# Kernel tuning notes

Measured on AMD Instinct MI355X. Metric: run time of the kernel, lower is better.

Reference implementation:

```python
import jax, jax.numpy as jnp
import numpy as np

INPUT_SIZE = 224
B, C, H, W = 256, 3, 256, 256
KSIZE = 15
KHALF = KSIZE // 2


def setup_inputs() -> dict:
    key = jax.random.key(0)
    x = jax.random.uniform(key, (B, C, H, W), dtype=jnp.float32)
    return {"x": x}


def _rgb_to_hsv(img):  # img [B,3,Hs,Ws] -> (h,s,v) each [B,Hs,Ws]
    r, g, b = img[:, 0], img[:, 1], img[:, 2]
    maxc = jnp.maximum(jnp.maximum(r, g), b)
    minc = jnp.minimum(jnp.minimum(r, g), b)
    v = maxc
    d = maxc - minc
    s = jnp.where(maxc > 0, d / jnp.where(maxc > 0, maxc, 1.0), 0.0)
    dn = jnp.where(d > 0, d, 1.0)
    rc, gc, bc = (maxc - r) / dn, (maxc - g) / dn, (maxc - b) / dn
    h = jnp.where(maxc == r, bc - gc, jnp.where(maxc == g, 2.0 + rc - bc, 4.0 + gc - rc))
    h = jnp.where(d > 0, (h / 6.0) % 1.0, 0.0)
    return h, s, v


def _hsv_to_rgb(h, s, v):  # -> [B,3,Hs,Ws]
    i = jnp.floor(h * 6.0)
    f = h * 6.0 - i
    i = i.astype(jnp.int32) % 6
    p = v * (1.0 - s)
    q = v * (1.0 - s * f)
    t = v * (1.0 - s * (1.0 - f))
    conds = [i == 0, i == 1, i == 2, i == 3, i == 4, i == 5]
    r = jnp.select(conds, [v, q, p, p, t, v])
    g = jnp.select(conds, [t, v, v, q, p, p])
    b = jnp.select(conds, [p, p, t, v, v, q])
    return jnp.stack([r, g, b], axis=1)


def _gray(img):  # ITU-R 601 luma, keep channel dim
    w = jnp.array([0.2989, 0.587, 0.114], dtype=img.dtype).reshape(1, 3, 1, 1)
    return jnp.sum(img * w, axis=1, keepdims=True)


def _blur_axis(img, kern, axis):
    # img [B,C,S,S]; kern [B,KSIZE]; separable 1D gaussian along `axis` with reflect pad
    pad = [(0, 0)] * 4
    pad[axis] = (KHALF, KHALF)
    xp = jnp.pad(img, pad, mode='reflect')
    out = jnp.zeros_like(img)
    S = img.shape[axis]
    for k in range(KSIZE):  # fixed small loop, fuses under jit
        sl = jax.lax.slice_in_dim(xp, k, k + S, axis=axis)
        out = out + kern[:, k].reshape(B, 1, 1, 1) * sl
    return out


def _pipeline(x):
    key = jax.random.key(42)
    ks = jax.random.split(key, 10)

    # ---- RandomResizedCrop(scale=(0.8,1.0), ratio=(3/4,4/3), bicubic) ----
    area = (H * W) * jax.random.uniform(ks[0], (B,), minval=0.8, maxval=1.0)
    ratio = jnp.exp(jax.random.uniform(ks[1], (B,), minval=np.log(3.0 / 4.0), maxval=np.log(4.0 / 3.0)))
    cw = jnp.clip(jnp.round(jnp.sqrt(area * ratio)), 1.0, float(W))
    ch = jnp.clip(jnp.round(jnp.sqrt(area / ratio)), 1.0, float(H))
    i0 = jnp.floor(jax.random.uniform(ks[2], (B,)) * (H - ch + 1.0))
    j0 = jnp.floor(jax.random.uniform(ks[3], (B,)) * (W - cw + 1.0))
    sy, sx = INPUT_SIZE / ch, INPUT_SIZE / cw
    ty, tx = -i0 * sy, -j0 * sx

    def crop_resize(img, scale, trans):
        return jax.image.scale_and_translate(
            img, (C, INPUT_SIZE, INPUT_SIZE), (1, 2), scale, trans,
            method='cubic', antialias=True)

    xc = jax.vmap(crop_resize)(x, jnp.stack([sy, sx], -1), jnp.stack([ty, tx], -1))

    # ---- ColorJitter(0.1, 0.1, 0.1, 0.01), RandomApply p=0.8 ----
    bf = jax.random.uniform(ks[4], (B, 1, 1, 1), minval=0.9, maxval=1.1)
    cf = jax.random.uniform(ks[5], (B, 1, 1, 1), minval=0.9, maxval=1.1)
    sf = jax.random.uniform(ks[6], (B, 1, 1, 1), minval=0.9, maxval=1.1)
    hf = jax.random.uniform(ks[7], (B, 1, 1), minval=-0.01, maxval=0.01)

    xj = jnp.clip(xc * bf, 0.0, 1.0)                                      # brightness
    mean_gray = jnp.mean(_gray(xj), axis=(2, 3), keepdims=True)
    xj = jnp.clip(cf * xj + (1.0 - cf) * mean_gray, 0.0, 1.0)             # contrast
    xj = jnp.clip(sf * xj + (1.0 - sf) * _gray(xj), 0.0, 1.0)             # saturation
    h, s, v = _rgb_to_hsv(xj)                                             # hue
    xj = _hsv_to_rgb((h + hf) % 1.0, s, v)

    apply_cj = (jax.random.uniform(ks[8], (B, 1, 1, 1)) < 0.8)
    xj = jnp.where(apply_cj, xj, xc)

    # ---- GaussianBlur(kernel_size=15, sigma~U(0.1,2.0)), RandomApply p=0.5 ----
    kb = jax.random.split(ks[9], 2)
    sigma = jax.random.uniform(kb[0], (B,), minval=0.1, maxval=2.0)
    t = jnp.arange(KSIZE, dtype=jnp.float32) - KHALF
    kern = jnp.exp(-0.5 * (t[None, :] / sigma[:, None]) ** 2)
    kern = kern / jnp.sum(kern, axis=1, keepdims=True)                    # [B,15]
    xb = _blur_axis(_blur_axis(xj, kern, 2), kern, 3)
    apply_bl = (jax.random.uniform(kb[1], (B, 1, 1, 1)) < 0.5)
    return jnp.where(apply_bl, xb, xj)


def reference(x):
    return _pipeline(x)
```

## Files before the change

### kernel.cpp

```cpp
#include <hip/hip_runtime.h>
#include <cstdint>
#include <cstddef>


#define JAX_PARTITIONABLE 1

#define NB 256
#define NC 3
#define IH 256
#define IW 256
#define OS 224
#define PIX (OS * OS)
#define PSTRIDE 32
#define TROWS 16
#define LROWS 24
#define NTILE 14
#define CSTRIDE 28
#define YSTR 25

__device__ __forceinline__ float bf2f(unsigned short u) {
  return __uint_as_float(((unsigned)u) << 16);
}
__device__ __forceinline__ unsigned short f2bf(float f) {
  unsigned u = __float_as_uint(f);
  return (unsigned short)((u + 0x7FFFu + ((u >> 16) & 1u)) >> 16);
}

__device__ __forceinline__ void tf2x32(uint32_t k0, uint32_t k1,
                                       uint32_t x0, uint32_t x1,
                                       uint32_t& o0, uint32_t& o1) {
  uint32_t ks[3] = {k0, k1, k0 ^ k1 ^ 0x1BD11BDAu};
  uint32_t a = x0 + ks[0], b = x1 + ks[1];
  const int R[2][4] = {{13, 15, 26, 6}, {17, 29, 16, 24}};
  #pragma unroll
  for (int i = 0; i < 5; ++i) {
    #pragma unroll
    for (int j = 0; j < 4; ++j) {
      int r = R[i & 1][j];
      a += b;
      b = (b << r) | (b >> (32 - r));
      b ^= a;
    }
    a += ks[(i + 1) % 3];
    b += ks[(i + 2) % 3] + (uint32_t)(i + 1);
  }
  o0 = a; o1 = b;
}

__device__ __forceinline__ float bits_to_u01(uint32_t bits) {
  uint32_t fb = (bits >> 9) | 0x3f800000u;
  return __uint_as_float(fb) - 1.0f;
}

__device__ __forceinline__ float u01_n(uint32_t k0, uint32_t k1, uint32_t i, uint32_t N) {
#if JAX_PARTITIONABLE
  uint32_t a, b; tf2x32(k0, k1, 0u, i, a, b);
  return bits_to_u01(a ^ b);
#else
  uint32_t half = N >> 1;
  uint32_t a, b;
  if (i < half) { tf2x32(k0, k1, i, half + i, a, b); return bits_to_u01(a); }
  tf2x32(k0, k1, i - half, i, a, b); return bits_to_u01(b);
#endif
}

__device__ __forceinline__ float junif(uint32_t k0, uint32_t k1, uint32_t i, uint32_t N,
                                       float mn, float mx) {
  float u = u01_n(k0, k1, i, N);
  float d = __fsub_rn(mx, mn);
  float r = __fadd_rn(__fmul_rn(u, d), mn);
  return fmaxf(mn, r);
}

__global__ __launch_bounds__(256) void k_params(float* __restrict__ prm) {
  int b = threadIdx.x;
  if (b >= NB) return;
  uint32_t ks[10][2];
#if JAX_PARTITIONABLE
  for (int j = 0; j < 10; ++j) tf2x32(0u, 42u, 0u, (uint32_t)j, ks[j][0], ks[j][1]);
#else
  {
    uint32_t flat[20];
    for (int j = 0; j < 10; ++j) {
      uint32_t a, bb; tf2x32(0u, 42u, (uint32_t)j, (uint32_t)(10 + j), a, bb);
      flat[j] = a; flat[10 + j] = bb;
    }
    for (int j = 0; j < 10; ++j) { ks[j][0] = flat[2 * j]; ks[j][1] = flat[2 * j + 1]; }
  }
#endif
  float* P = prm + b * PSTRIDE;

  float uarea = junif(ks[0][0], ks[0][1], b, NB, 0.8f, 1.0f);
  float area  = __fmul_rn(65536.0f, uarea);
  float lmn = (float)(-0.28768207245178085);
  float lmx = (float)( 0.28768207245178085);
  float ur  = junif(ks[1][0], ks[1][1], b, NB, lmn, lmx);
  float ratio = (float)exp((double)ur);

  float cw = rintf(__fsqrt_rn(__fmul_rn(area, ratio)));
  cw = fminf(fmaxf(cw, 1.0f), 256.0f);
  float ch = rintf(__fsqrt_rn(__fdiv_rn(area, ratio)));
  ch = fminf(fmaxf(ch, 1.0f), 256.0f);

  float ui = u01_n(ks[2][0], ks[2][1], b, NB);
  float uj = u01_n(ks[3][0], ks[3][1], b, NB);
  float i0 = floorf(__fmul_rn(ui, __fadd_rn(__fsub_rn(256.0f, ch), 1.0f)));
  float j0 = floorf(__fmul_rn(uj, __fadd_rn(__fsub_rn(256.0f, cw), 1.0f)));

  float sy = __fdiv_rn(224.0f, ch), sx = __fdiv_rn(224.0f, cw);
  float ty = -__fmul_rn(i0, sy),   tx = -__fmul_rn(j0, sx);
  float inv_sy = __fdiv_rn(1.0f, sy), inv_sx = __fdiv_rn(1.0f, sx);
  P[0] = inv_sy;
  P[1] = __fmul_rn(ty, inv_sy);
  P[2] = fmaxf(inv_sy, 1.0f);
  P[3] = inv_sx;
  P[4] = __fmul_rn(tx, inv_sx);
  P[5] = fmaxf(inv_sx, 1.0f);

  P[6] = junif(ks[4][0], ks[4][1], b, NB, 0.9f, 1.1f);
  P[7] = junif(ks[5][0], ks[5][1], b, NB, 0.9f, 1.1f);
  P[8] = junif(ks[6][0], ks[6][1], b, NB, 0.9f, 1.1f);
  P[9] = junif(ks[7][0], ks[7][1], b, NB, -0.01f, 0.01f);
  P[10] = (u01_n(ks[8][0], ks[8][1], b, NB) < 0.8f) ? 1.0f : 0.0f;

  uint32_t kb0[2], kb1[2];
#if JAX_PARTITIONABLE
  tf2x32(ks[9][0], ks[9][1], 0u, 0u, kb0[0], kb0[1]);
  tf2x32(ks[9][0], ks[9][1], 0u, 1u, kb1[0], kb1[1]);
#else
  {
    uint32_t f0, s0, f1, s1;
    tf2x32(ks[9][0], ks[9][1], 0u, 2u, f0, s0);
    tf2x32(ks[9][0], ks[9][1], 1u, 3u, f1, s1);
    kb0[0] = f0; kb0[1] = f1; kb1[0] = s0; kb1[1] = s1;
  }
#endif
  float sg = junif(kb0[0], kb0[1], b, NB, 0.1f, 2.0f);
  P[11] = (u01_n(kb1[0], kb1[1], b, NB) < 0.5f) ? 1.0f : 0.0f;

  float e[15]; float ssum = 0.0f;
  for (int k = 0; k < 15; ++k) {
    float t = (float)k - 7.0f;
    float z = t / sg;
    e[k] = expf(-0.5f * (z * z));
    ssum += e[k];
  }
  for (int k = 0; k < 15; ++k) P[12 + k] = e[k] / ssum;
}

__device__ __forceinline__ float keys_cubic(float x) {
  float o = ((1.5f * x - 2.5f) * x) * x + 1.0f;
  if (x >= 1.0f) o = ((-0.5f * x + 2.5f) * x - 4.0f) * x + 2.0f;
  if (x >= 2.0f) o = 0.0f;
  return o;
}

__global__ __launch_bounds__(224) void k_weights(const float* __restrict__ prm,
                                                 float* __restrict__ wtab) {
  int o = threadIdx.x;
  int dim = blockIdx.x & 1;
  int b = blockIdx.x >> 1;
  const float* P = prm + b * PSTRIDE;
  float inv = dim ? P[3] : P[0];
  float ti  = dim ? P[4] : P[1];
  float ks  = dim ? P[5] : P[2];
  float sf = ((float)o + 0.5f) * inv - ti - 0.5f;
  float r = 2.0f * ks;
  int i0 = max(0, (int)ceilf(sf - r));
  int i1 = min(255, (int)floorf(sf + r));
  int n = i1 - i0 + 1; if (n > 6) n = 6;
  float w[6]; float tot = 0.0f;
  #pragma unroll
  for (int j = 0; j < 6; ++j) {
    float v = 0.0f;
    if (j < n) { float d = fabsf(sf - (float)(i0 + j)) / ks; v = keys_cubic(d); }
    w[j] = v; tot += v;
  }
  float ri = (fabsf(tot) > 1.1920929e-4f) ? (1.0f / tot) : 0.0f;
  float* W = wtab + ((size_t)(b * 2 + dim) * 224 + o) * 8;
  #pragma unroll
  for (int j = 0; j < 6; ++j) W[j] = w[j] * ri;
  W[6] = (float)i0;
  W[7] = (float)n;
}

__global__ __launch_bounds__(256) void k_resize(const float* __restrict__ x,
                                                unsigned short* __restrict__ xcj,
                                                float* __restrict__ rowsum,
                                                const float* __restrict__ prm,
                                                const float* __restrict__ wtab) {
  int blk = blockIdx.x;
  int tile = blk % NTILE;
  int c = (blk / NTILE) % NC;
  int b = blk / (NTILE * NC);
  int t = threadIdx.x;
  int oyb = tile * TROWS;
  const float* P = prm + b * PSTRIDE;
  const float* wty = wtab + ((size_t)(b * 2) * 224 + oyb) * 8;

  __shared__ __align__(16) float s_mem[256 * CSTRIDE];
  __shared__ __align__(16) float s_wyl[TROWS * 8];
  __shared__ float wsum[4];

  if (t < TROWS * 8) s_wyl[t] = wty[t];

  int base = (int)wty[6];

  {
    const float* src = x + (size_t)(b * NC + c) * IH * IW + t;
    float* colp = s_mem + t * CSTRIDE;
    #pragma unroll
    for (int k = 0; k < 6; ++k) {
      float4 v;
      v.x = src[(size_t)min(base + 4 * k + 0, IH - 1) * IW];
      v.y = src[(size_t)min(base + 4 * k + 1, IH - 1) * IW];
      v.z = src[(size_t)min(base + 4 * k + 2, IH - 1) * IW];
      v.w = src[(size_t)min(base + 4 * k + 3, IH - 1) * IW];
      *(float4*)(colp + 4 * k) = v;
    }
  }
  __syncthreads();

  float xr[LROWS];
  #pragma unroll
  for (int r = 0; r < LROWS; ++r) xr[r] = 0.0f;
  if (t < OS) {
    const float4* W4 = (const float4*)(wtab + ((size_t)(b * 2 + 1) * 224 + t) * 8);
    float4 wA = W4[0], wB = W4[1];
    int ix0 = (int)wB.z;
    #pragma unroll
    for (int j = 0; j < 6; ++j) {
      float wj = (j == 0) ? wA.x : (j == 1) ? wA.y : (j == 2) ? wA.z
               : (j == 3) ? wA.w : (j == 4) ? wB.x : wB.y;
      const float* colp = s_mem + (ix0 + j) * CSTRIDE;
      #pragma unroll
      for (int k = 0; k < 6; ++k) {
        float4 f = *(const float4*)(colp + 4 * k);
        xr[4 * k + 0] += wj * f.x;
        xr[4 * k + 1] += wj * f.y;
        xr[4 * k + 2] += wj * f.z;
        xr[4 * k + 3] += wj * f.w;
      }
    }
  }
  __syncthreads();

  {
    float* colq = s_mem + t * YSTR;
    #pragma unroll
    for (int r = 0; r < LROWS; ++r) colq[r] = xr[r];
  }
  __syncthreads();

  float bfac = P[6];
  float psum = 0.0f;
  bool act = (t < OS);
  unsigned short* dst = xcj + ((size_t)(b * NC + c) * OS + oyb) * OS + t;
  const float* colq = s_mem + t * YSTR;
  #pragma unroll 2
  for (int i = 0; i < TROWS; ++i) {
    float4 a = *(const float4*)&s_wyl[i * 8];
    float4 h = *(const float4*)&s_wyl[i * 8 + 4];
    int ry0 = (int)h.z - base;
    const float* p = colq + ry0;
    float acc = a.x * p[0] + a.y * p[1] + a.z * p[2]
              + a.w * p[3] + h.x * p[4] + h.y * p[5];
    if (act) {
      dst[(size_t)i * OS] = f2bf(acc);
      psum += fminf(fmaxf(acc * bfac, 0.0f), 1.0f);
    }
  }
  for (int off = 32; off > 0; off >>= 1) psum += __shfl_down(psum, off, 64);
  int wid = t >> 6, lane = t & 63;
  if (lane == 0) wsum[wid] = psum;
  __syncthreads();
  if (t == 0) rowsum[blk] = wsum[0] + wsum[1] + wsum[2] + wsum[3];
}

__global__ __launch_bounds__(64) void k_means(const float* __restrict__ rowsum,
                                              float* __restrict__ means) {
  int b = blockIdx.x, t = threadIdx.x;
  float acc = 0.0f;
  if (t < NC * NTILE) {
    int c = t / NTILE;
    float w = (c == 0) ? 0.2989f : ((c == 1) ? 0.587f : 0.114f);
    acc = w * rowsum[b * NC * NTILE + t];
  }
  for (int off = 32; off > 0; off >>= 1) acc += __shfl_down(acc, off, 64);
  if (t == 0) means[b] = acc / (float)PIX;
}

__device__ __forceinline__ float clip01(float x) { return fminf(fmaxf(x, 0.0f), 1.0f); }
__device__ __forceinline__ float fmod1(float x)  { return x - floorf(x); }

__device__ __forceinline__ void jitter_px(float& r, float& g, float& bb,
                                          float mg, float bfac, float cfac,
                                          float sfac, float hfac) {
  r = clip01(r * bfac); g = clip01(g * bfac); bb = clip01(bb * bfac);
  r  = clip01(cfac * r  + (1.0f - cfac) * mg);
  g  = clip01(cfac * g  + (1.0f - cfac) * mg);
  bb = clip01(cfac * bb + (1.0f - cfac) * mg);
  float gray = 0.2989f * r + 0.587f * g + 0.114f * bb;
  r  = clip01(sfac * r  + (1.0f - sfac) * gray);
  g  = clip01(sfac * g  + (1.0f - sfac) * gray);
  bb = clip01(sfac * bb + (1.0f - sfac) * gray);
  float maxc = fmaxf(r, fmaxf(g, bb));
  float minc = fminf(r, fminf(g, bb));
  float v = maxc, d = maxc - minc;
  float s = (maxc > 0.0f) ? (d / maxc) : 0.0f;
  float dn = (d > 0.0f) ? d : 1.0f;
  float rc = (maxc - r) / dn, gc = (maxc - g) / dn, bc2 = (maxc - bb) / dn;
  float h = (maxc == r) ? (bc2 - gc)
          : ((maxc == g) ? (2.0f + rc - bc2) : (4.0f + gc - rc));
  h = (d > 0.0f) ? fmod1(h / 6.0f) : 0.0f;
  h = fmod1(h + hfac);
  float fi = floorf(h * 6.0f);
  float f = h * 6.0f - fi;
  int i = ((int)fi) % 6;
  float pp = v * (1.0f - s);
  float q  = v * (1.0f - s * f);
  float tt = v * (1.0f - s * (1.0f - f));
  switch (i) {
    case 0: r = v;  g = tt; bb = pp; break;
    case 1: r = q;  g = v;  bb = pp; break;
    case 2: r = pp; g = v;  bb = tt; break;
    case 3: r = pp; g = q;  bb = v;  break;
    case 4: r = tt; g = pp; bb = v;  break;
    default: r = v; g = pp; bb = q;  break;
  }
}

__global__ __launch_bounds__(256) void k_jitter(unsigned short* __restrict__ xcj,
                                                const float* __restrict__ means,
                                                const float* __restrict__ prm,
                                                float* __restrict__ out) {
  int idx = blockIdx.x * 256 + threadIdx.x;
  const int QPB = PIX / 4;
  if (idx >= NB * QPB) return;
  int b = idx / QPB, p4 = idx - b * QPB;
  const float* P = prm + b * PSTRIDE;
  float bfac = P[6], cfac = P[7], sfac = P[8], hfac = P[9];
  bool cj = P[10] != 0.0f;
  bool bl = P[11] != 0.0f;
  if (bl && !cj) return;
  size_t base4 = ((size_t)b * NC * PIX) / 4 + p4;
  ushort4* in4 = (ushort4*)xcj;
  ushort4 ru = in4[base4];
  ushort4 gu = in4[base4 + PIX / 4];
  ushort4 bu = in4[base4 + 2 * (PIX / 4)];
  float4 r4 = make_float4(bf2f(ru.x), bf2f(ru.y), bf2f(ru.z), bf2f(ru.w));
  float4 g4 = make_float4(bf2f(gu.x), bf2f(gu.y), bf2f(gu.z), bf2f(gu.w));
  float4 b4 = make_float4(bf2f(bu.x), bf2f(bu.y), bf2f(bu.z), bf2f(bu.w));
  if (cj) {
    float mg = means[b];
    float* rp = (float*)&r4; float* gp = (float*)&g4; float* bp = (float*)&b4;
    #pragma unroll
    for (int k = 0; k < 4; ++k) jitter_px(rp[k], gp[k], bp[k], mg, bfac, cfac, sfac, hfac);
  }
  if (bl) {
    ushort4 s;
    s.x = f2bf(r4.x); s.y = f2bf(r4.y); s.z = f2bf(r4.z); s.w = f2bf(r4.w);
    in4[base4] = s;
    s.x = f2bf(g4.x); s.y = f2bf(g4.y); s.z = f2bf(g4.z); s.w = f2bf(g4.w);
    in4[base4 + PIX / 4] = s;
    s.x = f2bf(b4.x); s.y = f2bf(b4.y); s.z = f2bf(b4.z); s.w = f2bf(b4.w);
    in4[base4 + 2 * (PIX / 4)] = s;
  } else {
    float4* dst4 = (float4*)out;
    dst4[base4] = r4;
    dst4[base4 + PIX / 4] = g4;
    dst4[base4 + 2 * (PIX / 4)] = b4;
  }
}

__global__ __launch_bounds__(256) void k_blur(const unsigned short* __restrict__ xcj,
                                              float* __restrict__ out,
                                              const float* __restrict__ prm) {
  int blk = blockIdx.x;
  int tile = blk % NTILE;
  int c = (blk / NTILE) % NC;
  int b = blk / (NTILE * NC);
  const float* P = prm + b * PSTRIDE;
  if (P[11] == 0.0f) return;
  int t = threadIdx.x;
  int oyb = tile * TROWS;

  __shared__ unsigned short s_in[TROWS + 14][228];
  __shared__ float s_mid[TROWS][226];
  __shared__ float s_k[15];
  if (t < 15) s_k[t] = P[12 + t];

  const unsigned short* plane = xcj + (size_t)(b * NC + c) * PIX;
  float* oplane = out + (size_t)(b * NC + c) * PIX;

  {
    const int RQ = OS / 4;
    for (int f = t; f < (TROWS + 14) * RQ; f += 256) {
      int r = f / RQ, q = f - r * RQ;
      int yy = oyb - 7 + r;
      yy = (yy < 0) ? -yy : ((yy > OS - 1) ? (2 * (OS - 1) - yy) : yy);
      *(ushort4*)&s_in[r][4 * q] = *(const ushort4*)(plane + (size_t)yy * OS + 4 * q);
    }
  }
  __syncthreads();

  float w[15];
  #pragma unroll
  for (int k = 0; k < 15; ++k) w[k] = s_k[k];

  float acc[TROWS];
  #pragma unroll
  for (int i = 0; i < TROWS; ++i) acc[i] = 0.0f;
  if (t < OS) {
    #pragma unroll
    for (int r = 0; r < TROWS + 14; ++r) {
      float val = bf2f(s_in[r][t]);
      #pragma unroll
      for (int i = 0; i < TROWS; ++i) {
        if (i <= r && r - i <= 14) acc[i] += w[r - i] * val;
      }
    }
    #pragma unroll
    for (int i = 0; i < TROWS; ++i) s_mid[i][t] = acc[i];
  }
  __syncthreads();

  if (t < OS) {
    for (int i = 0; i < TROWS; ++i) {
      float a2 = 0.0f;
      #pragma unroll
      for (int k = 0; k < 15; ++k) {
        int xx = t - 7 + k;
        xx = (xx < 0) ? -xx : ((xx > OS - 1) ? (2 * (OS - 1) - xx) : xx);
        a2 += w[k] * s_mid[i][xx];
      }
      oplane[(size_t)(oyb + i) * OS + t] = a2;
    }
  }
}

extern "C" void kernel_launch(void* const* d_in, const int* in_sizes, int n_in,
                              void* d_out, int out_size, void* d_ws, size_t ws_size,
                              hipStream_t stream) {
  const float* x = (const float*)d_in[0];
  float* out = (float*)d_out;
  char* ws = (char*)d_ws;

  float* prm    = (float*)ws;
  float* rowsum = (float*)(ws + 32768);
  float* means  = (float*)(ws + 75776);
  float* wtab   = (float*)(ws + 76800);
  unsigned short* xcj = (unsigned short*)(ws + 3746816);

  k_params<<<1, 256, 0, stream>>>(prm);
  k_weights<<<NB * 2, 224, 0, stream>>>(prm, wtab);

  int nblk = NB * NC * NTILE;
  k_resize<<<nblk, 256, 0, stream>>>(x, xcj, rowsum, prm, wtab);
  k_means<<<NB, 64, 0, stream>>>(rowsum, means);

  int nquad = NB * (PIX / 4);
  k_jitter<<<(nquad + 255) / 256, 256, 0, stream>>>(xcj, means, prm, out);

  k_blur<<<nblk, 256, 0, stream>>>(xcj, out, prm);
}
```

Before: 170.8 us.

## Restructure horizontal blur pass with padded smem rows and float4 outputs

Result: slower. 184.2 us (+7.8%).

```diff
diff --git a/kernel.cpp b/kernel.cpp
--- a/kernel.cpp
+++ b/kernel.cpp
@@ -17,6 +17,7 @@
 #define NTILE 14
 #define CSTRIDE 28
 #define YSTR 25
+#define BSTR 240
 
 __device__ __forceinline__ float bf2f(unsigned short u) {
   return __uint_as_float(((unsigned)u) << 16);
@@ -199,10 +200,7 @@
   const float* wty = wtab + ((size_t)(b * 2) * 224 + oyb) * 8;
 
   __shared__ __align__(16) float s_mem[256 * CSTRIDE];
-  __shared__ __align__(16) float s_wyl[TROWS * 8];
   __shared__ float wsum[4];
-
-  if (t < TROWS * 8) s_wyl[t] = wty[t];
 
   int base = (int)wty[6];
 
@@ -259,8 +257,8 @@
   const float* colq = s_mem + t * YSTR;
   #pragma unroll 2
   for (int i = 0; i < TROWS; ++i) {
-    float4 a = *(const float4*)&s_wyl[i * 8];
-    float4 h = *(const float4*)&s_wyl[i * 8 + 4];
+    float4 a = *(const float4*)(wty + i * 8);
+    float4 h = *(const float4*)(wty + i * 8 + 4);
     int ry0 = (int)h.z - base;
     const float* p = colq + ry0;
     float acc = a.x * p[0] + a.y * p[1] + a.z * p[2]
@@ -386,9 +384,11 @@
   int oyb = tile * TROWS;
 
   __shared__ unsigned short s_in[TROWS + 14][228];
-  __shared__ float s_mid[TROWS][226];
-  __shared__ float s_k[15];
-  if (t < 15) s_k[t] = P[12 + t];
+  __shared__ __align__(16) float s_mid[TROWS][BSTR];
+
+  float w[15];
+  #pragma unroll
+  for (int k = 0; k < 15; ++k) w[k] = P[12 + k];
 
   const unsigned short* plane = xcj + (size_t)(b * NC + c) * PIX;
   float* oplane = out + (size_t)(b * NC + c) * PIX;
@@ -404,14 +404,10 @@
   }
   __syncthreads();
 
-  float w[15];
-  #pragma unroll
-  for (int k = 0; k < 15; ++k) w[k] = s_k[k];
-
-  float acc[TROWS];
-  #pragma unroll
-  for (int i = 0; i < TROWS; ++i) acc[i] = 0.0f;
   if (t < OS) {
+    float acc[TROWS];
+    #pragma unroll
+    for (int i = 0; i < TROWS; ++i) acc[i] = 0.0f;
     #pragma unroll
     for (int r = 0; r < TROWS + 14; ++r) {
       float val = bf2f(s_in[r][t]);
@@ -421,20 +417,36 @@
       }
     }
     #pragma unroll
-    for (int i = 0; i < TROWS; ++i) s_mid[i][t] = acc[i];
-  }
-  __syncthreads();
-
-  if (t < OS) {
     for (int i = 0; i < TROWS; ++i) {
-      float a2 = 0.0f;
+      s_mid[i][8 + t] = acc[i];
+      if (t >= 1 && t <= 7)     s_mid[i][8 - t] = acc[i];
+      if (t >= 216 && t <= 222) s_mid[i][454 - t] = acc[i];
+    }
+  }
+  __syncthreads();
+
+  #pragma unroll 1
+  for (int it = 0; it < 4; ++it) {
+    int f = it * 256 + t;
+    if (f < TROWS * 56) {
+      int r = f / 56, q = f - r * 56;
+      const float* row = &s_mid[r][0];
+      float v[20];
+      *(float4*)&v[0]  = *(const float4*)(row + 4 * q);
+      *(float4*)&v[4]  = *(const float4*)(row + 4 * q + 4);
+      *(float4*)&v[8]  = *(const float4*)(row + 4 * q + 8);
+      *(float4*)&v[12] = *(const float4*)(row + 4 * q + 12);
+      *(float4*)&v[16] = *(const float4*)(row + 4 * q + 16);
+      float4 o;
+      float* op = (float*)&o;
       #pragma unroll
-      for (int k = 0; k < 15; ++k) {
-        int xx = t - 7 + k;
-        xx = (xx < 0) ? -xx : ((xx > OS - 1) ? (2 * (OS - 1) - xx) : xx);
-        a2 += w[k] * s_mid[i][xx];
+      for (int m = 0; m < 4; ++m) {
+        float acc = 0.0f;
+        #pragma unroll
+        for (int k = 0; k < 15; ++k) acc += w[k] * v[m + k + 1];
+        op[m] = acc;
       }
-      oplane[(size_t)(oyb + i) * OS + t] = a2;
+      *(float4*)(oplane + (size_t)(oyb + r) * OS + 4 * q) = o;
     }
   }
 }
```
